# Optimization experiments

Measured on AMD Instinct MI355X. Metric: run time of the kernel, lower is better.

Reference implementation:

```python
import jax, jax.numpy as jnp
import numpy as np

N_HEADS = 4
T_OUT = 24  # total T; y has T - t_in steps


def setup_inputs() -> dict:
    key = jax.random.key(0)
    k1, k2, k3, k4 = jax.random.split(key, 4)
    B, t_in, N, C, K = 2, 12, 10000, 16, 17  # K = k + 1 (self)
    x = jax.random.normal(k1, (B, t_in, N, C), dtype=jnp.float32)
    nearest_nodes = jax.random.randint(k2, (N, K), 0, N, dtype=jnp.int32)
    nearest_dists = jax.random.uniform(k3, (N, K), dtype=jnp.float32)
    shrink_w = jax.random.normal(k4, (T_OUT - t_in, t_in * N_HEADS), dtype=jnp.float32) * 0.1
    shrink_b = jnp.zeros((T_OUT - t_in,), dtype=jnp.float32)
    return {"x": x, "nearest_nodes": nearest_nodes, "nearest_dists": nearest_dists,
            "shrink_w": shrink_w, "shrink_b": shrink_b}


def reference(x, nearest_nodes, nearest_dists, shrink_w, shrink_b):
    B, t_in, N, C = x.shape
    H = N_HEADS
    # sigma = nearest_dists.max() / sigma_ratio, with sigma_ratio = 1
    sigma = jnp.max(nearest_dists)
    lam = jnp.arange(1, H + 1, dtype=x.dtype) / H  # (H,)
    # distance weights per head: (N, K, H)
    w = jnp.exp(-(nearest_dists[..., None] ** 2) * lam / (sigma ** 2))
    w = jnp.where((nearest_nodes == -1)[..., None], 0.0, w)
    w = jnp.where(w < 1e-8, 0.0, w)
    # pad node at index N; -1 neighbors map to pad (weight already zero)
    pad_x = jnp.concatenate([x, jnp.zeros_like(x[:, :, :1])], axis=2)  # (B,T,N+1,C)
    idx = jnp.where(nearest_nodes == -1, N, nearest_nodes)  # (N, K)
    g = pad_x[:, :, idx]  # (B, t_in, N, K, C) neighbor gather
    # weighted reduce over neighbor axis -> (B, t_in, N, H, C)
    agg = jnp.einsum('btnkc,nkh->btnhc', g, w)
    # (B, N, C, t_in*H)
    a = jnp.transpose(agg, (0, 2, 4, 1, 3)).reshape(B, N, C, t_in * H)
    y = a @ shrink_w.T + shrink_b  # (B, N, C, T - t_in)
    y = jnp.transpose(y, (0, 3, 1, 2))  # (B, T - t_in, N, C)
    y = jax.nn.selu(y)  # CustomActivationFunction default mode='selu'
    return jnp.concatenate([x, y], axis=1)  # (B, T, N, C)
```

## Files before the change

### kernel.cpp

```cpp
#include <hip/hip_runtime.h>
#include <hip/hip_bf16.h>
#include <math.h>

#define NB      2
#define T_IN    12
#define T_OUT_  24
#define O_OUT   12
#define NN      10000
#define CC      16
#define KK      17
#define HH      4
#define JJ      48
#define PL      24
#define XCHN    40
#define CHN     250
#define XBLK    (PL * XCHN)
#define SBLK    167
#define GW      4
#define GBLK    (NN / GW)
#define PSTR    68
#define ANS     (PL * PSTR)

__device__ __forceinline__ unsigned int f2bf(float f) {
    union { float f; unsigned int u; } v; v.f = f;
    unsigned int r = v.u + 0x7FFFu + ((v.u >> 16) & 1u);
    return r >> 16;
}
__device__ __forceinline__ float bf_lo(unsigned int u) {
    union { unsigned int u; float f; } v; v.u = u << 16; return v.f;
}
__device__ __forceinline__ float bf_hi(unsigned int u) {
    union { unsigned int u; float f; } v; v.u = u & 0xffff0000u; return v.f;
}

__device__ __forceinline__ void wave_fence() {
#if __has_builtin(__builtin_amdgcn_wave_barrier)
    __builtin_amdgcn_wave_barrier();
#else
    __syncthreads();
#endif
}

__global__ __launch_bounds__(256) void setup_kernel(
    const float* __restrict__ x,
    const float* __restrict__ dists, int ndists,
    float* __restrict__ out,
    unsigned short* __restrict__ xt,
    int* __restrict__ sigma_bits)
{
    const int tid = threadIdx.x;
    if (blockIdx.x < XBLK) {
        const int p  = blockIdx.x / XCHN;
        const int ch = blockIdx.x % XCHN;
        const int b = p / T_IN, t = p % T_IN;
        const int n0 = ch * CHN;
        const float* xp = x + (long)(p * NN + n0) * CC;
        float* op = out + (long)((b * T_OUT_ + t) * NN + n0) * CC;
        uint2* xtp = (uint2*)xt + (long)n0 * (PL * 4) + p * 4;
        for (int i = tid; i < CHN * 4; i += 256) {
            const int nl = i >> 2, q = i & 3;
            const float4 v = *(const float4*)(xp + i * 4);
            *(float4*)(op + i * 4) = v;
            uint2 pk;
            pk.x = f2bf(v.x) | (f2bf(v.y) << 16);
            pk.y = f2bf(v.z) | (f2bf(v.w) << 16);
            xtp[(long)nl * (PL * 4) + q] = pk;
        }
    } else {
        const int sb = blockIdx.x - XBLK;
        float m = 0.0f;
        const int nv4 = ndists >> 2;
        const float4* d4 = (const float4*)dists;
        for (int i = sb * 256 + tid; i < nv4; i += SBLK * 256) {
            float4 v = d4[i];
            m = fmaxf(fmaxf(m, fmaxf(v.x, v.y)), fmaxf(v.z, v.w));
        }
        for (int i = (nv4 << 2) + sb * 256 + tid; i < ndists; i += SBLK * 256)
            m = fmaxf(m, dists[i]);
        #pragma unroll
        for (int off = 32; off > 0; off >>= 1)
            m = fmaxf(m, __shfl_down(m, off, 64));
        __shared__ float sm[4];
        int lane = tid & 63, wid = tid >> 6;
        if (lane == 0) sm[wid] = m;
        __syncthreads();
        if (tid == 0) {
            float mm = fmaxf(fmaxf(sm[0], sm[1]), fmaxf(sm[2], sm[3]));
            atomicMax(sigma_bits, __float_as_int(mm));
        }
    }
}

__global__ __launch_bounds__(256) void fused_kernel(
    const unsigned short* __restrict__ xt,
    const int*   __restrict__ nodes,
    const float* __restrict__ dists,
    const int*   __restrict__ sigma_bits,
    const float* __restrict__ Wm,
    const float* __restrict__ bias,
    float* __restrict__ out)
{
    const int tid  = threadIdx.x;
    const int wave = tid >> 6;
    const int lane = tid & 63;
    const int n0   = blockIdx.x * GW;

    __shared__ float W_s[O_OUT * JJ];
    __shared__ float b_s[O_OUT];
    __shared__ uint4 lrec[GW * KK];
    __shared__ float a_s[GW * ANS];

    for (int i = tid; i < O_OUT * JJ; i += 256) W_s[i] = Wm[i];
    if (tid < O_OUT) b_s[tid] = bias[tid];
    if (tid < GW * KK) {
        const float sigma  = __int_as_float(*sigma_bits);
        const float inv_s2 = 1.0f / (sigma * sigma);
        const int   nd = nodes[n0 * KK + tid];
        const float dd = dists[n0 * KK + tid];
        const float e1 = expf(-dd * dd * inv_s2 * 0.25f);
        float w0 = e1, w1 = e1 * e1, w2 = w1 * e1, w3 = w1 * w1;
        if (nd == -1) { w0 = w1 = w2 = w3 = 0.f; }
        if (w0 < 1e-8f) w0 = 0.f;
        if (w1 < 1e-8f) w1 = 0.f;
        if (w2 < 1e-8f) w2 = 0.f;
        if (w3 < 1e-8f) w3 = 0.f;
        uint4 rec;
        rec.x = (unsigned)(((nd < 0) ? 0 : nd) * (PL * CC * 2));
        rec.y = f2bf(w0) | (f2bf(w1) << 16);
        rec.z = f2bf(w2) | (f2bf(w3) << 16);
        rec.w = 0;
        lrec[tid] = rec;
    }
    __syncthreads();

    const int rb = wave * KK;
    float* abase = a_s + wave * ANS;
    if (lane < 48) {
        const char* xtb = (const char*)xt;
        float acc[HH][8];
        #pragma unroll
        for (int h = 0; h < HH; ++h)
            #pragma unroll
            for (int j = 0; j < 8; ++j) acc[h][j] = 0.f;

        #pragma unroll
        for (int k = 0; k < KK; ++k) {
            const uint4 rec = lrec[rb + k];
            const uint4 gv  = *(const uint4*)(xtb + rec.x + (lane << 4));
            const float w0 = bf_lo(rec.y), w1 = bf_hi(rec.y);
            const float w2 = bf_lo(rec.z), w3 = bf_hi(rec.z);
            float g[8];
            g[0] = bf_lo(gv.x); g[1] = bf_hi(gv.x);
            g[2] = bf_lo(gv.y); g[3] = bf_hi(gv.y);
            g[4] = bf_lo(gv.z); g[5] = bf_hi(gv.z);
            g[6] = bf_lo(gv.w); g[7] = bf_hi(gv.w);
            #pragma unroll
            for (int j = 0; j < 8; ++j) {
                acc[0][j] += g[j] * w0;
                acc[1][j] += g[j] * w1;
                acc[2][j] += g[j] * w2;
                acc[3][j] += g[j] * w3;
            }
        }

        const int plane = lane >> 1;
        const int oct   = lane & 1;
        float* ap = abase + plane * PSTR + oct * 32;
        #pragma unroll
        for (int j = 0; j < 8; ++j)
            *(float4*)(ap + j * 4) =
                make_float4(acc[0][j], acc[1][j], acc[2][j], acc[3][j]);
    }
    wave_fence();

    const float kScale = 1.0507009873554805f;
    const float kAlpha = 1.6732632423543772f;
    const int n = n0 + wave;
    const int c = lane & 15;
    const int q = lane >> 4;
    #pragma unroll
    for (int r = 0; r < 6; ++r) {
        const int rr = r * 4 + q;
        const int o  = rr % O_OUT;
        const int b  = rr / O_OUT;
        const float* ab = abase + (b * T_IN) * PSTR + c * 4;
        const float* wb = W_s + o * JJ;
        float y = b_s[o];
        #pragma unroll
        for (int t = 0; t < T_IN; ++t) {
            const float4 av = *(const float4*)(ab + t * PSTR);
            const float4 wv = *(const float4*)(wb + t * 4);
            y += av.x * wv.x + av.y * wv.y + av.z * wv.z + av.w * wv.w;
        }
        y = (y > 0.0f) ? kScale * y : kScale * kAlpha * (__expf(y) - 1.0f);
        out[((long)(b * T_OUT_ + T_IN + o) * NN + n) * CC + c] = y;
    }
}

extern "C" void kernel_launch(void* const* d_in, const int* in_sizes, int n_in,
                              void* d_out, int out_size, void* d_ws, size_t ws_size,
                              hipStream_t stream) {
    const float* x     = (const float*)d_in[0];
    const int*   nodes = (const int*)  d_in[1];
    const float* dists = (const float*)d_in[2];
    const float* Wm    = (const float*)d_in[3];
    const float* bias  = (const float*)d_in[4];
    float* out = (float*)d_out;

    char* ws = (char*)d_ws;
    int*            sigma_bits = (int*)ws;
    unsigned short* xt         = (unsigned short*)(ws + 1024);

    const int ndists = in_sizes[2];
    setup_kernel<<<XBLK + SBLK, 256, 0, stream>>>(x, dists, ndists, out, xt,
                                                  sigma_bits);
    fused_kernel<<<GBLK, 256, 0, stream>>>(xt, nodes, dists, sigma_bits,
                                           Wm, bias, out);
}
```

Baseline: 111.6 us.

## Batch neighbor gathers up front, use packed float2 FMAs, reuse weights across batches

Splits the per-neighbor LDS record into separate index and weight arrays and issues all 17 neighbor gathers before any arithmetic, so the global loads are in flight together instead of one at a time. The accumulation is rewritten with 2-wide float vectors so the compiler can emit packed FMA instructions. The output projection is restructured so each lane computes 3 outputs for both batches, loading each weight vector once and sharing it across the two batches. The cost is many more live registers (17 uint4 gather results), which may lower occupancy.

```diff
diff --git a/kernel.cpp b/kernel.cpp
--- a/kernel.cpp
+++ b/kernel.cpp
@@ -21,6 +21,8 @@
 #define PSTR    68
 #define ANS     (PL * PSTR)
 
+typedef float v2f __attribute__((ext_vector_type(2)));
+
 __device__ __forceinline__ unsigned int f2bf(float f) {
     union { float f; unsigned int u; } v; v.f = f;
     unsigned int r = v.u + 0x7FFFu + ((v.u >> 16) & 1u);
@@ -31,6 +33,12 @@
 }
 __device__ __forceinline__ float bf_hi(unsigned int u) {
     union { unsigned int u; float f; } v; v.u = u & 0xffff0000u; return v.f;
+}
+__device__ __forceinline__ v2f bfpair(unsigned int u) {
+    v2f r;
+    r.x = bf_lo(u);
+    r.y = bf_hi(u);
+    return r;
 }
 
 __device__ __forceinline__ void wave_fence() {
@@ -105,10 +113,11 @@
     const int lane = tid & 63;
     const int n0   = blockIdx.x * GW;
 
-    __shared__ float W_s[O_OUT * JJ];
-    __shared__ float b_s[O_OUT];
-    __shared__ uint4 lrec[GW * KK];
-    __shared__ float a_s[GW * ANS];
+    __shared__ float    W_s[O_OUT * JJ];
+    __shared__ float    b_s[O_OUT];
+    __shared__ unsigned lidx[GW * KK];
+    __shared__ uint2    lw2[GW * KK];
+    __shared__ float    a_s[GW * ANS];
 
     for (int i = tid; i < O_OUT * JJ; i += 256) W_s[i] = Wm[i];
     if (tid < O_OUT) b_s[tid] = bias[tid];
@@ -124,12 +133,9 @@
         if (w1 < 1e-8f) w1 = 0.f;
         if (w2 < 1e-8f) w2 = 0.f;
         if (w3 < 1e-8f) w3 = 0.f;
-        uint4 rec;
-        rec.x = (unsigned)(((nd < 0) ? 0 : nd) * (PL * CC * 2));
-        rec.y = f2bf(w0) | (f2bf(w1) << 16);
-        rec.z = f2bf(w2) | (f2bf(w3) << 16);
-        rec.w = 0;
-        lrec[tid] = rec;
+        lidx[tid] = (unsigned)(((nd < 0) ? 0 : nd) * (PL * CC * 2));
+        lw2[tid]  = make_uint2(f2bf(w0) | (f2bf(w1) << 16),
+                               f2bf(w2) | (f2bf(w3) << 16));
     }
     __syncthreads();
 
@@ -137,29 +143,35 @@
     float* abase = a_s + wave * ANS;
     if (lane < 48) {
         const char* xtb = (const char*)xt;
-        float acc[HH][8];
+        uint4 gv[KK];
+        #pragma unroll
+        for (int k = 0; k < KK; ++k)
+            gv[k] = *(const uint4*)(xtb + lidx[rb + k] + (lane << 4));
+
+        v2f acc[HH][4];
         #pragma unroll
         for (int h = 0; h < HH; ++h)
             #pragma unroll
-            for (int j = 0; j < 8; ++j) acc[h][j] = 0.f;
+            for (int p = 0; p < 4; ++p) acc[h][p] = (v2f){0.f, 0.f};
 
         #pragma unroll
         for (int k = 0; k < KK; ++k) {
-            const uint4 rec = lrec[rb + k];
-            const uint4 gv  = *(const uint4*)(xtb + rec.x + (lane << 4));
-            const float w0 = bf_lo(rec.y), w1 = bf_hi(rec.y);
-            const float w2 = bf_lo(rec.z), w3 = bf_hi(rec.z);
-            float g[8];
-            g[0] = bf_lo(gv.x); g[1] = bf_hi(gv.x);
-            g[2] = bf_lo(gv.y); g[3] = bf_hi(gv.y);
-            g[4] = bf_lo(gv.z); g[5] = bf_hi(gv.z);
-            g[6] = bf_lo(gv.w); g[7] = bf_hi(gv.w);
+            const uint2 wp = lw2[rb + k];
+            const v2f vw0 = {bf_lo(wp.x), bf_lo(wp.x)};
+            const v2f vw1 = {bf_hi(wp.x), bf_hi(wp.x)};
+            const v2f vw2 = {bf_lo(wp.y), bf_lo(wp.y)};
+            const v2f vw3 = {bf_hi(wp.y), bf_hi(wp.y)};
+            v2f g[4];
+            g[0] = bfpair(gv[k].x);
+            g[1] = bfpair(gv[k].y);
+            g[2] = bfpair(gv[k].z);
+            g[3] = bfpair(gv[k].w);
             #pragma unroll
-            for (int j = 0; j < 8; ++j) {
-                acc[0][j] += g[j] * w0;
-                acc[1][j] += g[j] * w1;
-                acc[2][j] += g[j] * w2;
-                acc[3][j] += g[j] * w3;
+            for (int p = 0; p < 4; ++p) {
+                acc[0][p] += g[p] * vw0;
+                acc[1][p] += g[p] * vw1;
+                acc[2][p] += g[p] * vw2;
+                acc[3][p] += g[p] * vw3;
             }
         }
 
@@ -167,9 +179,11 @@
         const int oct   = lane & 1;
         float* ap = abase + plane * PSTR + oct * 32;
         #pragma unroll
-        for (int j = 0; j < 8; ++j)
-            *(float4*)(ap + j * 4) =
-                make_float4(acc[0][j], acc[1][j], acc[2][j], acc[3][j]);
+        for (int j = 0; j < 8; ++j) {
+            const int p = j >> 1, e = j & 1;
+            *(float4*)(ap + j * 4) = make_float4(acc[0][p][e], acc[1][p][e],
+                                                 acc[2][p][e], acc[3][p][e]);
+        }
     }
     wave_fence();
 
@@ -177,24 +191,33 @@
     const float kAlpha = 1.6732632423543772f;
     const int n = n0 + wave;
     const int c = lane & 15;
-    const int q = lane >> 4;
+    const int d = lane >> 4;
+    float y[3][NB];
     #pragma unroll
-    for (int r = 0; r < 6; ++r) {
-        const int rr = r * 4 + q;
-        const int o  = rr % O_OUT;
-        const int b  = rr / O_OUT;
-        const float* ab = abase + (b * T_IN) * PSTR + c * 4;
-        const float* wb = W_s + o * JJ;
-        float y = b_s[o];
-        #pragma unroll
-        for (int t = 0; t < T_IN; ++t) {
-            const float4 av = *(const float4*)(ab + t * PSTR);
-            const float4 wv = *(const float4*)(wb + t * 4);
-            y += av.x * wv.x + av.y * wv.y + av.z * wv.z + av.w * wv.w;
-        }
-        y = (y > 0.0f) ? kScale * y : kScale * kAlpha * (__expf(y) - 1.0f);
-        out[((long)(b * T_OUT_ + T_IN + o) * NN + n) * CC + c] = y;
-    }
+    for (int i = 0; i < 3; ++i) {
+        const float bv = b_s[d * 3 + i];
+        y[i][0] = bv; y[i][1] = bv;
+    }
+    #pragma unroll
+    for (int t = 0; t < T_IN; ++t) {
+        const float4 a0 = *(const float4*)(abase + t * PSTR + c * 4);
+        const float4 a1 = *(const float4*)(abase + (T_IN + t) * PSTR + c * 4);
+        #pragma unroll
+        for (int i = 0; i < 3; ++i) {
+            const float4 wv = *(const float4*)(W_s + (d * 3 + i) * JJ + t * 4);
+            y[i][0] += a0.x * wv.x + a0.y * wv.y + a0.z * wv.z + a0.w * wv.w;
+            y[i][1] += a1.x * wv.x + a1.y * wv.y + a1.z * wv.z + a1.w * wv.w;
+        }
+    }
+    #pragma unroll
+    for (int i = 0; i < 3; ++i)
+        #pragma unroll
+        for (int b = 0; b < NB; ++b) {
+            float v = y[i][b];
+            v = (v > 0.0f) ? kScale * v : kScale * kAlpha * (__expf(v) - 1.0f);
+            const int o = d * 3 + i;
+            out[((long)(b * T_OUT_ + T_IN + o) * NN + n) * CC + c] = v;
+        }
 }
 
 extern "C" void kernel_launch(void* const* d_in, const int* in_sizes, int n_in,
```

Result: no change. 111.8 us (median of 2 runs) (+0.1%).
